# Performance work log

Hardware: AMD Instinct MI355X
Metric: run time of the kernel (lower is better)

Reference implementation:

```python
import jax, jax.numpy as jnp
import numpy as np

NUM_HEADS = 12

def setup_inputs() -> dict:
    key = jax.random.key(0)
    ks = jax.random.split(key, 8)
    B, N, C, H, R = 8, 1024, 768, NUM_HEADS, 4
    hd = C // H
    x = jax.random.normal(ks[0], (B, N, C), dtype=jnp.float32)
    Wqkv = jax.random.normal(ks[1], (3 * C, C), dtype=jnp.float32) * (C ** -0.5)
    Wproj = jax.random.normal(ks[2], (C, C), dtype=jnp.float32) * (C ** -0.5)
    bproj = jnp.zeros((C,), dtype=jnp.float32)
    Aq = jax.random.normal(ks[3], (hd, R), dtype=jnp.float32) * (hd ** -0.5)
    Bq = jax.random.normal(ks[4], (R, hd), dtype=jnp.float32) * (R ** -0.5)
    Av = jax.random.normal(ks[5], (hd, R), dtype=jnp.float32) * (hd ** -0.5)
    Bv = jax.random.normal(ks[6], (R, hd), dtype=jnp.float32) * (R ** -0.5)
    return {"x": x, "Wqkv": Wqkv, "Wproj": Wproj, "bproj": bproj,
            "Aq": Aq, "Bq": Bq, "Av": Av, "Bv": Bv}

def reference(x, Wqkv, Wproj, bproj, Aq, Bq, Av, Bv):
    B, N, C = x.shape
    H = NUM_HEADS
    hd = C // H
    scale = hd ** -0.5
    # QKV projection: [B,N,3C] -> [3,B,H,N,hd]
    qkv = (x @ Wqkv.T).reshape(B, N, 3, H, hd).transpose(2, 0, 3, 1, 4)
    q, k, v = qkv[0], qkv[1], qkv[2]
    # LoRA low-rank deltas on Q and V
    q = q + (q @ Aq) @ Bq
    v = v + (v @ Av) @ Bv
    # Attention scores [B,H,N,N]
    attn = jnp.einsum('bhnd,bhmd->bhnm', q, k) * scale
    attn = jax.nn.softmax(attn, axis=-1)
    out = jnp.einsum('bhnm,bhmd->bhnd', attn, v)  # [B,H,N,hd]
    out = out.transpose(0, 2, 1, 3).reshape(B, N, C)
    return out @ Wproj.T + bproj
```

## Files before the change

### kernel.cpp

```cpp
#include <hip/hip_runtime.h>

#define DEV __device__ __forceinline__

typedef _Float16 f16x8 __attribute__((ext_vector_type(8)));
typedef _Float16 f16x4 __attribute__((ext_vector_type(4)));
typedef float f32x4 __attribute__((ext_vector_type(4)));
typedef float f32x16 __attribute__((ext_vector_type(16)));
typedef unsigned int u32x4 __attribute__((ext_vector_type(4)));
typedef unsigned int u32x2 __attribute__((ext_vector_type(2)));

DEV void glds16(const void* g, void* l) {
    __builtin_amdgcn_global_load_lds(
        (const __attribute__((address_space(1))) void*)g,
        (__attribute__((address_space(3))) void*)l, 16, 0, 0);
}

DEV unsigned pkh(float lo, float hi) {
    return __builtin_bit_cast(unsigned, __builtin_amdgcn_cvt_pkrtz(lo, hi));
}

__global__ __launch_bounds__(256) void cast_f32_f16(const float* __restrict__ src,
                                                    _Float16* __restrict__ dst, int n4) {
    const int i = blockIdx.x * 256 + threadIdx.x;
    if (i >= n4) return;
    const float4 v = ((const float4*)src)[i];
    f16x4 o = { (_Float16)v.x, (_Float16)v.y, (_Float16)v.z, (_Float16)v.w };
    *(f16x4*)(dst + (size_t)i * 4) = o;
}

__global__ __launch_bounds__(256) void prep_w(const float* __restrict__ W,
                                              const float* __restrict__ Aq,
                                              const float* __restrict__ Bq,
                                              const float* __restrict__ Av,
                                              const float* __restrict__ Bv,
                                              _Float16* __restrict__ Wb) {
    const int bx = blockIdx.x;
    const int sec = bx / 12;
    const int h = bx - sec * 12;
    const float* Am = sec ? Av : Aq;
    const float* Bm = sec ? Bv : Bq;
    const int base = sec ? (1536 + h * 64) : (h * 64);
    const float scale = sec ? 1.0f : (0.125f * 1.4426950408889634f);
    const int c = blockIdx.y * 256 + threadIdx.x;
    float t0 = 0.f, t1 = 0.f, t2 = 0.f, t3 = 0.f;
    for (int j = 0; j < 64; ++j) {
        const float w = W[(size_t)(base + j) * 768 + c];
        t0 += Am[j * 4 + 0] * w;
        t1 += Am[j * 4 + 1] * w;
        t2 += Am[j * 4 + 2] * w;
        t3 += Am[j * 4 + 3] * w;
    }
    for (int i = 0; i < 64; ++i) {
        const float w = W[(size_t)(base + i) * 768 + c];
        const float val = w + t0 * Bm[i] + t1 * Bm[64 + i] + t2 * Bm[128 + i] + t3 * Bm[192 + i];
        Wb[(size_t)(base + i) * 768 + c] = (_Float16)(val * scale);
    }
}

template <int EPI, int MF, int GX, int GY>
__global__ __launch_bounds__(256) void gemm_nt(const _Float16* __restrict__ A,
                                               const _Float16* __restrict__ B,
                                               int Kdim, void* __restrict__ Cout,
                                               const float* __restrict__ bias) {
    constexpr int BM = MF * 32;
    constexpr int XB = GX / 8;
    __shared__ __align__(16) _Float16 As[BM * 64];
    __shared__ __align__(16) _Float16 Bs[128 * 64];
    const int tid = threadIdx.x;
    const int lane = tid & 63, wid = tid >> 6;
    const int l15 = lane & 15, l16 = lane >> 4;
    const int id = blockIdx.x;
    const int xcd = id & 7, c = id >> 3;
    const int bx = xcd * XB + (c % XB), by = c / XB;
    const int m0 = bx * BM, n0 = by << 7;
    const int wm = (wid >> 1) * (MF * 16), wn = (wid & 1) << 6;

    auto stage = [&](int k0) {
#pragma unroll
        for (int rr = 0; rr < MF; ++rr) {
            const int slot = (rr << 8) + tid;
            const int row = slot >> 3, sl = slot & 7;
            glds16(A + (size_t)(m0 + row) * Kdim + k0 + ((sl ^ (row & 7)) << 3),
                   (char*)As + (((rr << 8) + (wid << 6)) << 4));
        }
#pragma unroll
        for (int rr = 0; rr < 4; ++rr) {
            const int slot = (rr << 8) + tid;
            const int row = slot >> 3, sl = slot & 7;
            glds16(B + (size_t)(n0 + row) * Kdim + k0 + ((sl ^ (row & 7)) << 3),
                   (char*)Bs + (((rr << 8) + (wid << 6)) << 4));
        }
    };

    f32x4 acc[MF][4];
#pragma unroll
    for (int i = 0; i < MF; ++i)
#pragma unroll
        for (int j = 0; j < 4; ++j) acc[i][j] = (f32x4){0.f, 0.f, 0.f, 0.f};

    stage(0);
    __syncthreads();

    for (int k0 = 0; k0 < Kdim; k0 += 64) {
        f16x8 af[2][MF], bf[2][4];
#pragma unroll
        for (int kh = 0; kh < 2; ++kh) {
#pragma unroll
            for (int i = 0; i < MF; ++i) {
                const int ra = wm + i * 16 + l15;
                af[kh][i] = *(const f16x8*)((const char*)As + ra * 128 +
                                            ((((kh << 2) + l16) ^ (ra & 7)) << 4));
            }
#pragma unroll
            for (int j = 0; j < 4; ++j) {
                const int rb = wn + j * 16 + l15;
                bf[kh][j] = *(const f16x8*)((const char*)Bs + rb * 128 +
                                            ((((kh << 2) + l16) ^ (rb & 7)) << 4));
            }
        }
        __syncthreads();
        if (k0 + 64 < Kdim) stage(k0 + 64);
        __builtin_amdgcn_sched_barrier(0);
#pragma unroll
        for (int kh = 0; kh < 2; ++kh)
#pragma unroll
            for (int i = 0; i < MF; ++i)
#pragma unroll
                for (int j = 0; j < 4; ++j)
                    acc[i][j] = __builtin_amdgcn_mfma_f32_16x16x32_f16(af[kh][i], bf[kh][j],
                                                                       acc[i][j], 0, 0, 0);
        __syncthreads();
    }

    if (EPI == 0) {
        _Float16* qkv = (_Float16*)Cout;
#pragma unroll
        for (int j = 0; j < 4; ++j) {
            const int col = n0 + wn + j * 16 + l15;
            const int which = col / 768;
            const int rem = col - which * 768;
            const int hh = rem >> 6, d = rem & 63;
#pragma unroll
            for (int i = 0; i < MF; ++i) {
                const int rowb = m0 + wm + i * 16 + (l16 << 2);
                const int b = rowb >> 10, n = rowb & 1023;
                const int b12h = b * 12 + hh;
                if (which == 2) {
                    f16x4 pk = { (_Float16)acc[i][j][0], (_Float16)acc[i][j][1],
                                 (_Float16)acc[i][j][2], (_Float16)acc[i][j][3] };
                    *(f16x4*)(qkv + 12582912 +
                              ((((size_t)b12h * 64 + (n >> 4)) * 64 + d) << 4) + (n & 15)) = pk;
                } else if (which == 1) {
                    const size_t hb = 6291456 + ((size_t)b12h << 16);
#pragma unroll
                    for (int r = 0; r < 4; ++r) {
                        const int kv = n + r;
                        const int off = ((((kv >> 5) << 2) + (d >> 4)) << 9) +
                                        ((((kv & 31) << 1) + ((d >> 3) & 1)) << 3) + (d & 7);
                        qkv[hb + off] = (_Float16)acc[i][j][r];
                    }
                } else {
#pragma unroll
                    for (int r = 0; r < 4; ++r)
                        qkv[(((size_t)b12h << 10) + n + r) * 64 + d] = (_Float16)acc[i][j][r];
                }
            }
        }
    } else {
        float* out = (float*)Cout;
#pragma unroll
        for (int j = 0; j < 4; ++j) {
            const int col = n0 + wn + j * 16 + l15;
            const float bv = bias[col];
#pragma unroll
            for (int i = 0; i < MF; ++i)
#pragma unroll
                for (int r = 0; r < 4; ++r) {
                    const int row = m0 + wm + i * 16 + (l16 << 2) + r;
                    out[(size_t)row * 768 + col] = acc[i][j][r] + bv;
                }
        }
    }
}

__global__ __launch_bounds__(512) void attn_kernel(const _Float16* __restrict__ Qg,
                                                   const _Float16* __restrict__ K4g,
                                                   const _Float16* __restrict__ V4g,
                                                   _Float16* __restrict__ AO) {
    __shared__ float lds_o[4][64][32];
    __shared__ float2 lds_ml[4][32];

    const int tid = threadIdx.x, lane = tid & 63, wid = tid >> 6;
    const int l31 = lane & 31, hi = lane >> 5;
    const int wq = wid & 3, kvhalf = wid >> 2;
    const int bh = blockIdx.x;
    const int q = (blockIdx.y << 7) + (wq << 5) + l31;
    const int tbase = kvhalf << 4;
    const _Float16* K4h = K4g + ((size_t)bh << 16);
    const _Float16* V4h = V4g + ((size_t)bh << 16);

    f16x8 qf[4];
#pragma unroll
    for (int kd = 0; kd < 4; ++kd)
        qf[kd] = *(const f16x8*)(Qg + (((size_t)bh << 10) + q) * 64 + kd * 16 + hi * 8);

    f32x16 o0, o1;
#pragma unroll
    for (int j = 0; j < 16; ++j) { o0[j] = 0.f; o1[j] = 0.f; }
    float m_run = -INFINITY, l_run = 0.f;

    f16x8 kf[4], va[4], vb[4];
#pragma unroll
    for (int kd = 0; kd < 4; ++kd)
        kf[kd] = *(const f16x8*)(K4h + ((size_t)((tbase << 2) + kd) << 9) +
                                 (((l31 << 1) + hi) << 3));
#pragma unroll
    for (int dh = 0; dh < 2; ++dh)
#pragma unroll
        for (int ks = 0; ks < 2; ++ks)
            va[dh * 2 + ks] = *(const f16x8*)(V4h + ((size_t)((tbase << 1) + ks) << 10) +
                                              ((dh * 32 + l31) << 4) + hi * 8);

    auto body = [&](int kt, f16x8* vc, f16x8* vn) {
        f32x16 st;
#pragma unroll
        for (int j = 0; j < 16; ++j) st[j] = 0.f;
#pragma unroll
        for (int kd = 0; kd < 4; ++kd)
            st = __builtin_amdgcn_mfma_f32_32x32x16_f16(kf[kd], qf[kd], st, 0, 0, 0);

        const int tn = tbase + ((kt + 1) & 15);
#pragma unroll
        for (int kd = 0; kd < 4; ++kd)
            kf[kd] = *(const f16x8*)(K4h + ((size_t)((tn << 2) + kd) << 9) +
                                     (((l31 << 1) + hi) << 3));
#pragma unroll
        for (int dh = 0; dh < 2; ++dh)
#pragma unroll
            for (int ks = 0; ks < 2; ++ks)
                vn[dh * 2 + ks] = *(const f16x8*)(V4h + ((size_t)((tn << 1) + ks) << 10) +
                                                  ((dh * 32 + l31) << 4) + hi * 8);
        __builtin_amdgcn_sched_barrier(0);

        float tr[8];
#pragma unroll
        for (int j = 0; j < 8; ++j) tr[j] = fmaxf(st[2 * j], st[2 * j + 1]);
#pragma unroll
        for (int j = 0; j < 4; ++j) tr[j] = fmaxf(tr[j], tr[j + 4]);
        float mx = fmaxf(fmaxf(tr[0], tr[2]), fmaxf(tr[1], tr[3]));
        mx = fmaxf(mx, __shfl_xor(mx, 32));
        if (!__all(mx <= m_run + 8.f)) {
            const float mnew = fmaxf(m_run, mx);
            const float fac = __builtin_amdgcn_exp2f(m_run - mnew);
            l_run *= fac;
#pragma unroll
            for (int j = 0; j < 16; ++j) { o0[j] *= fac; o1[j] *= fac; }
            m_run = mnew;
        }
        float p[16];
#pragma unroll
        for (int j = 0; j < 16; ++j) p[j] = __builtin_amdgcn_exp2f(st[j] - m_run);
        float sr[8];
#pragma unroll
        for (int j = 0; j < 8; ++j) sr[j] = p[2 * j] + p[2 * j + 1];
#pragma unroll
        for (int j = 0; j < 4; ++j) sr[j] = sr[j] + sr[j + 4];
        float sum = (sr[0] + sr[2]) + (sr[1] + sr[3]);
        sum += __shfl_xor(sum, 32);
        l_run += sum;

        const unsigned a0 = pkh(p[0], p[1]),   a1 = pkh(p[2], p[3]);
        const unsigned a2 = pkh(p[4], p[5]),   a3 = pkh(p[6], p[7]);
        const unsigned a4 = pkh(p[8], p[9]),   a5 = pkh(p[10], p[11]);
        const unsigned a6 = pkh(p[12], p[13]), a7 = pkh(p[14], p[15]);
        const unsigned b0 = (unsigned)__shfl_xor((int)a0, 32);
        const unsigned b1 = (unsigned)__shfl_xor((int)a1, 32);
        const unsigned b2 = (unsigned)__shfl_xor((int)a2, 32);
        const unsigned b3 = (unsigned)__shfl_xor((int)a3, 32);
        const unsigned b4 = (unsigned)__shfl_xor((int)a4, 32);
        const unsigned b5 = (unsigned)__shfl_xor((int)a5, 32);
        const unsigned b6 = (unsigned)__shfl_xor((int)a6, 32);
        const unsigned b7 = (unsigned)__shfl_xor((int)a7, 32);
        const u32x4 w0 = { hi ? b2 : a0, hi ? b3 : a1, hi ? a2 : b0, hi ? a3 : b1 };
        const u32x4 w1 = { hi ? b6 : a4, hi ? b7 : a5, hi ? a6 : b4, hi ? a7 : b5 };
        const f16x8 pa0 = __builtin_bit_cast(f16x8, w0);
        const f16x8 pa1 = __builtin_bit_cast(f16x8, w1);

        o0 = __builtin_amdgcn_mfma_f32_32x32x16_f16(vc[0], pa0, o0, 0, 0, 0);
        o0 = __builtin_amdgcn_mfma_f32_32x32x16_f16(vc[1], pa1, o0, 0, 0, 0);
        o1 = __builtin_amdgcn_mfma_f32_32x32x16_f16(vc[2], pa0, o1, 0, 0, 0);
        o1 = __builtin_amdgcn_mfma_f32_32x32x16_f16(vc[3], pa1, o1, 0, 0, 0);
    };

#pragma unroll 1
    for (int k2 = 0; k2 < 8; ++k2) {
        body(2 * k2,     va, vb);
        body(2 * k2 + 1, vb, va);
    }

    if (kvhalf) {
#pragma unroll
        for (int g = 0; g < 4; ++g) {
            *(f32x4*)&lds_o[wq][lane][4 * g] =
                (f32x4){o0[4 * g + 0], o0[4 * g + 1], o0[4 * g + 2], o0[4 * g + 3]};
            *(f32x4*)&lds_o[wq][lane][16 + 4 * g] =
                (f32x4){o1[4 * g + 0], o1[4 * g + 1], o1[4 * g + 2], o1[4 * g + 3]};
        }
        if (!hi) lds_ml[wq][l31] = make_float2(m_run, l_run);
    }
    __syncthreads();
    if (kvhalf) return;

    const float2 ml2 = lds_ml[wq][l31];
    const float M = fmaxf(m_run, ml2.x);
    const float f1 = __builtin_amdgcn_exp2f(m_run - M);
    const float f2 = __builtin_amdgcn_exp2f(ml2.x - M);
    const float inv = __builtin_amdgcn_rcpf(l_run * f1 + ml2.y * f2);
    const float c1 = f1 * inv, c2 = f2 * inv;

    const int b = bh / 12, h = bh - (bh / 12) * 12;
    _Float16* dst = AO + ((size_t)b * 1024 + q) * 768 + h * 64 + hi * 4;
#pragma unroll
    for (int g = 0; g < 4; ++g) {
        const f32x4 p0 = *(const f32x4*)&lds_o[wq][lane][4 * g];
        const f32x4 p1 = *(const f32x4*)&lds_o[wq][lane][16 + 4 * g];
        const u32x2 w0 = { pkh(o0[4 * g + 0] * c1 + p0[0] * c2, o0[4 * g + 1] * c1 + p0[1] * c2),
                           pkh(o0[4 * g + 2] * c1 + p0[2] * c2, o0[4 * g + 3] * c1 + p0[3] * c2) };
        *(f16x4*)(dst + g * 8) = __builtin_bit_cast(f16x4, w0);
        const u32x2 w1 = { pkh(o1[4 * g + 0] * c1 + p1[0] * c2, o1[4 * g + 1] * c1 + p1[1] * c2),
                           pkh(o1[4 * g + 2] * c1 + p1[2] * c2, o1[4 * g + 3] * c1 + p1[3] * c2) };
        *(f16x4*)(dst + 32 + g * 8) = __builtin_bit_cast(f16x4, w1);
    }
}

extern "C" void kernel_launch(void* const* d_in, const int* in_sizes, int n_in,
                              void* d_out, int out_size, void* d_ws, size_t ws_size,
                              hipStream_t stream) {
    (void)in_sizes; (void)n_in; (void)out_size; (void)ws_size;
    const float* x     = (const float*)d_in[0];
    const float* Wqkv  = (const float*)d_in[1];
    const float* Wproj = (const float*)d_in[2];
    const float* bproj = (const float*)d_in[3];
    const float* Aq    = (const float*)d_in[4];
    const float* Bq    = (const float*)d_in[5];
    const float* Av    = (const float*)d_in[6];
    const float* Bv    = (const float*)d_in[7];

    _Float16* Xb     = (_Float16*)d_ws;
    _Float16* Wqkvb  = Xb + 6291456;
    _Float16* Wprojb = Wqkvb + 1769472;
    _Float16* QKV    = Wprojb + 589824;
    _Float16* AO     = QKV + 18874368;
    float* out = (float*)d_out;

    cast_f32_f16<<<6144, 256, 0, stream>>>(x, Xb, 1572864);
    cast_f32_f16<<<576, 256, 0, stream>>>(Wqkv + 589824, Wqkvb + 589824, 147456);
    cast_f32_f16<<<576, 256, 0, stream>>>(Wproj, Wprojb, 147456);
    prep_w<<<dim3(24, 3), 256, 0, stream>>>(Wqkv, Aq, Bq, Av, Bv, Wqkvb);

    gemm_nt<0, 4, 64, 18><<<1152, 256, 0, stream>>>(Xb, Wqkvb, 768, (void*)QKV, nullptr);
    attn_kernel<<<dim3(96, 8), 512, 0, stream>>>(QKV, QKV + 6291456, QKV + 12582912, AO);
    gemm_nt<1, 2, 128, 6><<<768, 256, 0, stream>>>(AO, Wprojb, 768, (void*)out, bproj);
}
```

Before: 126.0 us.

## Software-pipeline QK^T one tile ahead of softmax and halve cross-half shuffles

Restructures the attention inner loop so the QK^T MFMA for tile t+1 is issued before the softmax of tile t, using two score accumulators (stA/stB) that alternate. V is no longer double-buffered; it is loaded at the start of each segment and K is prefetched two tiles ahead. The P-matrix lane exchange is cut from eight __shfl_xor calls to four by selecting which half to send before shuffling. Launch bounds now request 4 blocks per CU, which caps register use. The extra live score accumulator and the tighter register cap could cause spills, and the V load now sits closer to where it is consumed.

Result: slower. 134.9 us (+7.0%).

```diff
diff --git a/kernel.cpp b/kernel.cpp
--- a/kernel.cpp
+++ b/kernel.cpp
@@ -183,10 +183,10 @@
     }
 }
 
-__global__ __launch_bounds__(512) void attn_kernel(const _Float16* __restrict__ Qg,
-                                                   const _Float16* __restrict__ K4g,
-                                                   const _Float16* __restrict__ V4g,
-                                                   _Float16* __restrict__ AO) {
+__global__ __launch_bounds__(512, 4) void attn_kernel(const _Float16* __restrict__ Qg,
+                                                      const _Float16* __restrict__ K4g,
+                                                      const _Float16* __restrict__ V4g,
+                                                      _Float16* __restrict__ AO) {
     __shared__ float lds_o[4][64][32];
     __shared__ float2 lds_ml[4][32];
 
@@ -209,42 +209,48 @@
     for (int j = 0; j < 16; ++j) { o0[j] = 0.f; o1[j] = 0.f; }
     float m_run = -INFINITY, l_run = 0.f;
 
-    f16x8 kf[4], va[4], vb[4];
+    f16x8 kf[4], vf[4];
+    f32x16 stA, stB;
+
 #pragma unroll
     for (int kd = 0; kd < 4; ++kd)
         kf[kd] = *(const f16x8*)(K4h + ((size_t)((tbase << 2) + kd) << 9) +
                                  (((l31 << 1) + hi) << 3));
 #pragma unroll
-    for (int dh = 0; dh < 2; ++dh)
-#pragma unroll
-        for (int ks = 0; ks < 2; ++ks)
-            va[dh * 2 + ks] = *(const f16x8*)(V4h + ((size_t)((tbase << 1) + ks) << 10) +
-                                              ((dh * 32 + l31) << 4) + hi * 8);
-
-    auto body = [&](int kt, f16x8* vc, f16x8* vn) {
-        f32x16 st;
-#pragma unroll
-        for (int j = 0; j < 16; ++j) st[j] = 0.f;
+    for (int j = 0; j < 16; ++j) stA[j] = 0.f;
+#pragma unroll
+    for (int kd = 0; kd < 4; ++kd)
+        stA = __builtin_amdgcn_mfma_f32_32x32x16_f16(kf[kd], qf[kd], stA, 0, 0, 0);
+#pragma unroll
+    for (int kd = 0; kd < 4; ++kd)
+        kf[kd] = *(const f16x8*)(K4h + ((size_t)(((tbase + 1) << 2) + kd) << 9) +
+                                 (((l31 << 1) + hi) << 3));
+
+    auto seg = [&](int tl, f32x16& stC, f32x16& stN) {
+        const int tt = tbase + tl;
+#pragma unroll
+        for (int dh = 0; dh < 2; ++dh)
+#pragma unroll
+            for (int ks = 0; ks < 2; ++ks)
+                vf[dh * 2 + ks] = *(const f16x8*)(V4h + ((size_t)((tt << 1) + ks) << 10) +
+                                                  ((dh * 32 + l31) << 4) + hi * 8);
+
+#pragma unroll
+        for (int j = 0; j < 16; ++j) stN[j] = 0.f;
 #pragma unroll
         for (int kd = 0; kd < 4; ++kd)
-            st = __builtin_amdgcn_mfma_f32_32x32x16_f16(kf[kd], qf[kd], st, 0, 0, 0);
-
-        const int tn = tbase + ((kt + 1) & 15);
+            stN = __builtin_amdgcn_mfma_f32_32x32x16_f16(kf[kd], qf[kd], stN, 0, 0, 0);
+
+        const int tn = tbase + ((tl + 2) & 15);
 #pragma unroll
         for (int kd = 0; kd < 4; ++kd)
             kf[kd] = *(const f16x8*)(K4h + ((size_t)((tn << 2) + kd) << 9) +
                                      (((l31 << 1) + hi) << 3));
-#pragma unroll
-        for (int dh = 0; dh < 2; ++dh)
-#pragma unroll
-            for (int ks = 0; ks < 2; ++ks)
-                vn[dh * 2 + ks] = *(const f16x8*)(V4h + ((size_t)((tn << 1) + ks) << 10) +
-                                                  ((dh * 32 + l31) << 4) + hi * 8);
         __builtin_amdgcn_sched_barrier(0);
 
         float tr[8];
 #pragma unroll
-        for (int j = 0; j < 8; ++j) tr[j] = fmaxf(st[2 * j], st[2 * j + 1]);
+        for (int j = 0; j < 8; ++j) tr[j] = fmaxf(stC[2 * j], stC[2 * j + 1]);
 #pragma unroll
         for (int j = 0; j < 4; ++j) tr[j] = fmaxf(tr[j], tr[j + 4]);
         float mx = fmaxf(fmaxf(tr[0], tr[2]), fmaxf(tr[1], tr[3]));
@@ -259,7 +265,7 @@
         }
         float p[16];
 #pragma unroll
-        for (int j = 0; j < 16; ++j) p[j] = __builtin_amdgcn_exp2f(st[j] - m_run);
+        for (int j = 0; j < 16; ++j) p[j] = __builtin_amdgcn_exp2f(stC[j] - m_run);
         float sr[8];
 #pragma unroll
         for (int j = 0; j < 8; ++j) sr[j] = p[2 * j] + p[2 * j + 1];
@@ -273,29 +279,25 @@
         const unsigned a2 = pkh(p[4], p[5]),   a3 = pkh(p[6], p[7]);
         const unsigned a4 = pkh(p[8], p[9]),   a5 = pkh(p[10], p[11]);
         const unsigned a6 = pkh(p[12], p[13]), a7 = pkh(p[14], p[15]);
-        const unsigned b0 = (unsigned)__shfl_xor((int)a0, 32);
-        const unsigned b1 = (unsigned)__shfl_xor((int)a1, 32);
-        const unsigned b2 = (unsigned)__shfl_xor((int)a2, 32);
-        const unsigned b3 = (unsigned)__shfl_xor((int)a3, 32);
-        const unsigned b4 = (unsigned)__shfl_xor((int)a4, 32);
-        const unsigned b5 = (unsigned)__shfl_xor((int)a5, 32);
-        const unsigned b6 = (unsigned)__shfl_xor((int)a6, 32);
-        const unsigned b7 = (unsigned)__shfl_xor((int)a7, 32);
-        const u32x4 w0 = { hi ? b2 : a0, hi ? b3 : a1, hi ? a2 : b0, hi ? a3 : b1 };
-        const u32x4 w1 = { hi ? b6 : a4, hi ? b7 : a5, hi ? a6 : b4, hi ? a7 : b5 };
+        const unsigned s0 = (unsigned)__shfl_xor((int)(hi ? a0 : a2), 32);
+        const unsigned s1 = (unsigned)__shfl_xor((int)(hi ? a1 : a3), 32);
+        const unsigned s2 = (unsigned)__shfl_xor((int)(hi ? a4 : a6), 32);
+        const unsigned s3 = (unsigned)__shfl_xor((int)(hi ? a5 : a7), 32);
+        const u32x4 w0 = { hi ? s0 : a0, hi ? s1 : a1, hi ? a2 : s0, hi ? a3 : s1 };
+        const u32x4 w1 = { hi ? s2 : a4, hi ? s3 : a5, hi ? a6 : s2, hi ? a7 : s3 };
         const f16x8 pa0 = __builtin_bit_cast(f16x8, w0);
         const f16x8 pa1 = __builtin_bit_cast(f16x8, w1);
 
-        o0 = __builtin_amdgcn_mfma_f32_32x32x16_f16(vc[0], pa0, o0, 0, 0, 0);
-        o0 = __builtin_amdgcn_mfma_f32_32x32x16_f16(vc[1], pa1, o0, 0, 0, 0);
-        o1 = __builtin_amdgcn_mfma_f32_32x32x16_f16(vc[2], pa0, o1, 0, 0, 0);
-        o1 = __builtin_amdgcn_mfma_f32_32x32x16_f16(vc[3], pa1, o1, 0, 0, 0);
+        o0 = __builtin_amdgcn_mfma_f32_32x32x16_f16(vf[0], pa0, o0, 0, 0, 0);
+        o0 = __builtin_amdgcn_mfma_f32_32x32x16_f16(vf[1], pa1, o0, 0, 0, 0);
+        o1 = __builtin_amdgcn_mfma_f32_32x32x16_f16(vf[2], pa0, o1, 0, 0, 0);
+        o1 = __builtin_amdgcn_mfma_f32_32x32x16_f16(vf[3], pa1, o1, 0, 0, 0);
     };
 
 #pragma unroll 1
     for (int k2 = 0; k2 < 8; ++k2) {
-        body(2 * k2,     va, vb);
-        body(2 * k2 + 1, vb, va);
+        seg(2 * k2,     stA, stB);
+        seg(2 * k2 + 1, stB, stA);
     }
 
     if (kvhalf) {
```
